# Optimization experiments

Hardware: AMD Instinct MI355X
Metric: run time of the kernel (lower is better)

The kernel has to match this reference:

```python
import jax, jax.numpy as jnp
import numpy as np

N = 50000   # nodes
E = 800000  # edges (avg degree 16)
D = 128     # in_channels == out_channels == edge_dim
BN_EPS = 1e-5
LN_EPS = 1e-5


def setup_inputs() -> dict:
    key = jax.random.key(0)
    ks = jax.random.split(key, 8)
    s = 0.05
    return {
        "x": jax.random.normal(ks[0], (N, D), jnp.float32),
        "edge_index": jax.random.randint(ks[1], (2, E), 0, N, dtype=jnp.int64),
        "edge_attr": jax.random.normal(ks[2], (E, D), jnp.float32),
        "eps": jnp.zeros((), jnp.float32),                       # GINE train_eps init 0
        "We": jax.random.normal(ks[3], (D, D), jnp.float32) * s,  # edge lin: edge_dim -> in_channels
        "be": jnp.zeros((D,), jnp.float32),
        "W1": jax.random.normal(ks[4], (D, D), jnp.float32) * s,  # mlp first linear
        "b1": jnp.zeros((D,), jnp.float32),
        "bn_g": jnp.ones((D,), jnp.float32),
        "bn_b": jnp.zeros((D,), jnp.float32),
        "bn_rm": jnp.zeros((D,), jnp.float32),  # running mean (eval mode)
        "bn_rv": jnp.ones((D,), jnp.float32),   # running var (eval mode)
        "W2": jax.random.normal(ks[5], (D, D), jnp.float32) * s,  # mlp second linear
        "b2": jnp.zeros((D,), jnp.float32),
        "ln_g": jnp.ones((D,), jnp.float32),
        "ln_b": jnp.zeros((D,), jnp.float32),
    }


def reference(x, edge_index, edge_attr, eps, We, be, W1, b1,
              bn_g, bn_b, bn_rm, bn_rv, W2, b2, ln_g, ln_b):
    src, dst = edge_index[0], edge_index[1]  # PyG: message from x_j = x[src], aggregate at dst
    # GINE message: relu(x_j + Lin(edge_attr)); gather + elementwise
    msg = jax.nn.relu(x[src] + edge_attr @ We.T + be)            # [E, D]
    aggr = jax.ops.segment_sum(msg, dst, num_segments=N)         # scatter-sum -> [N, D]
    h = (1.0 + eps) * x + aggr
    # MLP: Linear -> BatchNorm1d (eval) -> ReLU -> (Dropout=id) -> Linear
    h = h @ W1.T + b1
    h = (h - bn_rm) * jax.lax.rsqrt(bn_rv + BN_EPS) * bn_g + bn_b
    h = jax.nn.relu(h)
    h = h @ W2.T + b2
    # LayerNorm over feature dim
    mu = jnp.mean(h, axis=-1, keepdims=True)
    var = jnp.mean(jnp.square(h - mu), axis=-1, keepdims=True)
    h = (h - mu) * jax.lax.rsqrt(var + LN_EPS) * ln_g + ln_b
    # residual (Identity since in==out) + relu; dropout is identity in eval
    return jax.nn.relu(h + x)
```

## Files before the change

kernel.cpp:

```cpp
#include <hip/hip_runtime.h>
#include <hip/hip_bf16.h>

#define D 128
#define LDK 136

typedef __bf16 bf16x8 __attribute__((ext_vector_type(8)));
typedef float  f32x4  __attribute__((ext_vector_type(4)));
typedef unsigned short u16;

__device__ __forceinline__ u16 f2bf(float f) {
    unsigned int u = __builtin_bit_cast(unsigned int, f);
    u = u + 0x7FFFu + ((u >> 16) & 1u);
    return (u16)(u >> 16);
}
__device__ __forceinline__ float bf2f(u16 h) {
    unsigned int u = ((unsigned int)h) << 16;
    return __builtin_bit_cast(float, u);
}
__device__ __forceinline__ unsigned int pk2(float lo, float hi) {
    return (unsigned int)f2bf(lo) | ((unsigned int)f2bf(hi) << 16);
}
__device__ __forceinline__ void cvt_store8(u16* dst, float4 a, float4 b) {
    uint4 v;
    v.x = pk2(a.x, a.y); v.y = pk2(a.z, a.w);
    v.z = pk2(b.x, b.y); v.w = pk2(b.z, b.w);
    *reinterpret_cast<uint4*>(dst) = v;
}
__device__ __forceinline__ void cvt_store8v(u16* dst, f32x4 a, f32x4 b) {
    uint4 v;
    v.x = pk2(a.x, a.y); v.y = pk2(a.z, a.w);
    v.z = pk2(b.x, b.y); v.w = pk2(b.z, b.w);
    *reinterpret_cast<uint4*>(dst) = v;
}
__device__ __forceinline__ bf16x8 cvt8r(f32x4 a, f32x4 b) {
    uint4 v;
    v.x = pk2(a.x, a.y); v.y = pk2(a.z, a.w);
    v.z = pk2(b.x, b.y); v.w = pk2(b.z, b.w);
    return __builtin_bit_cast(bf16x8, v);
}

__global__ __launch_bounds__(256)
void hist_kernel(const int* __restrict__ ei, int* __restrict__ counts, int E) {
    int e = blockIdx.x * 256 + threadIdx.x;
    if (e < E) atomicAdd(&counts[ei[E + e]], 1);
}

__global__ __launch_bounds__(256)
void scan_partial(const int* __restrict__ counts, int* __restrict__ bsum) {
    const int b = blockIdx.x, t = threadIdx.x;
    const int4 v = reinterpret_cast<const int4*>(counts + (size_t)b * 1024)[t];
    int s = v.x + v.y + v.z + v.w;
    #pragma unroll
    for (int off = 1; off < 64; off <<= 1) s += __shfl_xor(s, off);
    __shared__ int ws[4];
    if ((t & 63) == 0) ws[t >> 6] = s;
    __syncthreads();
    if (t == 0) bsum[b] = ws[0] + ws[1] + ws[2] + ws[3];
}
__global__ __launch_bounds__(256)
void scan_bsum(int* __restrict__ bsum, int nb) {
    const int t = threadIdx.x;
    int s = (t < nb) ? bsum[t] : 0;
    int inc = s;
    const int lane = t & 63;
    #pragma unroll
    for (int off = 1; off < 64; off <<= 1) {
        int v = __shfl_up(inc, off);
        if (lane >= off) inc += v;
    }
    __shared__ int ws[4];
    if (lane == 63) ws[t >> 6] = inc;
    __syncthreads();
    int woff = 0;
    for (int i = 0; i < (t >> 6); ++i) woff += ws[i];
    if (t < nb) bsum[t] = woff + inc - s;
}
__global__ __launch_bounds__(256)
void scan_emit(const int* __restrict__ counts, const int* __restrict__ bsum,
               int* __restrict__ offsets) {
    const int b = blockIdx.x, t = threadIdx.x;
    const int4 v = reinterpret_cast<const int4*>(counts + (size_t)b * 1024)[t];
    const int s = v.x + v.y + v.z + v.w;
    int inc = s;
    const int lane = t & 63;
    #pragma unroll
    for (int off = 1; off < 64; off <<= 1) {
        int u = __shfl_up(inc, off);
        if (lane >= off) inc += u;
    }
    __shared__ int ws[4];
    if (lane == 63) ws[t >> 6] = inc;
    __syncthreads();
    int woff = bsum[b];
    for (int i = 0; i < (t >> 6); ++i) woff += ws[i];
    int e0 = woff + inc - s;
    int4 o;
    o.x = e0; o.y = e0 + v.x; o.z = o.y + v.y; o.w = o.z + v.z;
    reinterpret_cast<int4*>(offsets + (size_t)b * 1024)[t] = o;
}

__global__ __launch_bounds__(256)
void scatter_kernel(const int* __restrict__ ei, int* __restrict__ off,
                    int4* __restrict__ rec, int E) {
    int e = blockIdx.x * 256 + threadIdx.x;
    if (e < E) {
        int s = ei[e];
        int d = ei[E + e];
        int p = atomicAdd(&off[d], 1);
        rec[p] = make_int4(e, s, d, 0);
    }
}

__global__ __launch_bounds__(256, 4)
void gine_edge_sorted(const float* __restrict__ x,
                      const float* __restrict__ ea,
                      const float* __restrict__ We,
                      const float* __restrict__ be,
                      const int4* __restrict__ rec,
                      float* __restrict__ aggr,
                      int E)
{
    __shared__ u16 buf[128][LDK];
    __shared__ int eid_lds[128];
    __shared__ int src_lds[128];
    __shared__ int dst_lds[128];

    const int tid = threadIdx.x;
    const int e0  = blockIdx.x * 128;

    {
        const int row = tid >> 1;
        const int c0  = (tid & 1) * 64;
        const float4* gw = reinterpret_cast<const float4*>(We + (size_t)row * D + c0);
        #pragma unroll
        for (int j = 0; j < 8; ++j) {
            float4 w0 = gw[2*j], w1 = gw[2*j+1];
            cvt_store8(&buf[row][c0 + 8*j], w0, w1);
        }
        if (tid < 128) {
            const int p = e0 + tid;
            if (p < E) {
                int4 r4 = rec[p];
                eid_lds[tid] = r4.x; src_lds[tid] = r4.y; dst_lds[tid] = r4.z;
            } else {
                eid_lds[tid] = 0; src_lds[tid] = 0; dst_lds[tid] = -1;
            }
        }
    }
    __syncthreads();

    const int wave = tid >> 6, lane = tid & 63;
    const int lhi = lane >> 4, llo = lane & 15;
    const int r0 = wave * 32;

    f32x4 acc[2][8];
    #pragma unroll
    for (int m = 0; m < 2; ++m)
        #pragma unroll
        for (int n = 0; n < 8; ++n) acc[m][n] = (f32x4){0.f, 0.f, 0.f, 0.f};

    const f32x4* pa = reinterpret_cast<const f32x4*>(ea + (size_t)eid_lds[r0 + llo] * D);
    const f32x4* pb = reinterpret_cast<const f32x4*>(ea + (size_t)eid_lds[r0 + 16 + llo] * D);

#define LOADG(G, KK) { const int f4_ = ((KK)*32 + lhi*8) >> 2;                 \
        G[0] = __builtin_nontemporal_load(pa + f4_);                           \
        G[1] = __builtin_nontemporal_load(pa + f4_ + 1);                       \
        G[2] = __builtin_nontemporal_load(pb + f4_);                           \
        G[3] = __builtin_nontemporal_load(pb + f4_ + 1); }
#define MFMAG(G, KK) { bf16x8 a0_ = cvt8r(G[0], G[1]);                         \
        bf16x8 a1_ = cvt8r(G[2], G[3]);                                        \
        const int k0_ = (KK)*32 + lhi*8;                                       \
        _Pragma("unroll")                                                      \
        for (int nf = 0; nf < 8; ++nf) {                                       \
            bf16x8 b_ = *reinterpret_cast<const bf16x8*>(&buf[nf*16 + llo][k0_]); \
            acc[0][nf] = __builtin_amdgcn_mfma_f32_16x16x32_bf16(a0_, b_, acc[0][nf], 0, 0, 0); \
            acc[1][nf] = __builtin_amdgcn_mfma_f32_16x16x32_bf16(a1_, b_, acc[1][nf], 0, 0, 0); \
        } }

    f32x4 gA[4], gB[4];
    LOADG(gA, 0); LOADG(gB, 1);
    MFMAG(gA, 0); LOADG(gA, 2);
    MFMAG(gB, 1); LOADG(gB, 3);
    MFMAG(gA, 2); MFMAG(gB, 3);
#undef LOADG
#undef MFMAG

    float bev[8];
    #pragma unroll
    for (int nf = 0; nf < 8; ++nf) bev[nf] = be[nf*16 + llo];

    __syncthreads();

    {
        const int row = tid >> 1;
        const int c0  = (tid & 1) * 64;
        const int s   = src_lds[row];
        const f32x4* gx = reinterpret_cast<const f32x4*>(x + (size_t)s * D + c0);
        f32x4 xa[8];
        #pragma unroll
        for (int j = 0; j < 8; ++j) xa[j] = gx[j];
        #pragma unroll
        for (int j = 0; j < 4; ++j)
            cvt_store8v(&buf[row][c0 + 8*j], xa[2*j], xa[2*j+1]);
        #pragma unroll
        for (int j = 0; j < 8; ++j) xa[j] = gx[8 + j];
        #pragma unroll
        for (int j = 0; j < 4; ++j)
            cvt_store8v(&buf[row][c0 + 32 + 8*j], xa[2*j], xa[2*j+1]);
    }
    __syncthreads();

    #pragma unroll
    for (int mf = 0; mf < 2; ++mf) {
        #pragma unroll
        for (int r = 0; r < 4; ++r) {
            const int row = r0 + mf*16 + lhi*4 + r;
            const bool valid = (e0 + row) < E;
            #pragma unroll
            for (int nf = 0; nf < 8; ++nf) {
                const int col = nf*16 + llo;
                const float v = acc[mf][nf][r] + bf2f(buf[row][col]) + bev[nf];
                buf[row][col] = valid ? f2bf(fmaxf(v, 0.0f)) : (u16)0;
            }
        }
    }
    __syncthreads();

    {
        const int c   = tid & 127;
        const int h   = tid >> 7;
        const int rlo = h * 64;
        float sum = 0.0f;
        int prev  = dst_lds[rlo];
        int start = rlo;
        #pragma unroll 4
        for (int r = rlo; r < rlo + 64; ++r) {
            const float v = bf2f(buf[r][c]);
            const int d = dst_lds[r];
            if (d != prev) {
                if (prev >= 0) {
                    float* p = &aggr[(size_t)prev * D + c];
                    if (start == rlo) atomicAdd(p, sum);
                    else              *p = sum;
                }
                sum = 0.0f; prev = d; start = r;
            }
            sum += v;
        }
        if (prev >= 0) atomicAdd(&aggr[(size_t)prev * D + c], sum);
    }
}

__global__ __launch_bounds__(256, 4)
void gine_edge(const float* __restrict__ x,
               const int* __restrict__ ei,
               const float* __restrict__ ea,
               const float* __restrict__ We,
               const float* __restrict__ be,
               float* __restrict__ aggr,
               int E)
{
    __shared__ u16 w_lds[128][LDK];
    __shared__ int sd_lds[2][128];

    const int tid = threadIdx.x;
    const int e0  = blockIdx.x * 128;

    {
        const int row = tid >> 1;
        const int c0  = (tid & 1) * 64;
        const float4* gw = reinterpret_cast<const float4*>(We + (size_t)row * D + c0);
        #pragma unroll
        for (int j = 0; j < 8; ++j) {
            float4 w0 = gw[2*j], w1 = gw[2*j+1];
            cvt_store8(&w_lds[row][c0 + 8*j], w0, w1);
        }
        const int r = tid & 127, which = tid >> 7;
        int erow = e0 + r;
        sd_lds[which][r] = (erow < E) ? ei[(size_t)which * E + erow] : 0;
    }
    __syncthreads();

    const int wave = tid >> 6, lane = tid & 63;
    const int lhi = lane >> 4, llo = lane & 15;
    const int r0 = wave * 32;

    f32x4 acc[2][8];
    #pragma unroll
    for (int m = 0; m < 2; ++m)
        #pragma unroll
        for (int n = 0; n < 8; ++n) acc[m][n] = (f32x4){0.f, 0.f, 0.f, 0.f};

    int ra = e0 + r0 + llo;      if (ra >= E) ra = E - 1;
    int rb = e0 + r0 + 16 + llo; if (rb >= E) rb = E - 1;
    const f32x4* pa = reinterpret_cast<const f32x4*>(ea + (size_t)ra * D);
    const f32x4* pb = reinterpret_cast<const f32x4*>(ea + (size_t)rb * D);

    #pragma unroll
    for (int kk = 0; kk < 4; ++kk) {
        const int k0 = kk * 32 + lhi * 8;
        const int f4 = k0 >> 2;
        f32x4 u0 = __builtin_nontemporal_load(pa + f4);
        f32x4 u1 = __builtin_nontemporal_load(pa + f4 + 1);
        f32x4 v0 = __builtin_nontemporal_load(pb + f4);
        f32x4 v1 = __builtin_nontemporal_load(pb + f4 + 1);
        bf16x8 a0 = cvt8r(u0, u1);
        bf16x8 a1 = cvt8r(v0, v1);
        #pragma unroll
        for (int nf = 0; nf < 8; ++nf) {
            bf16x8 b = *reinterpret_cast<const bf16x8*>(&w_lds[nf*16 + llo][k0]);
            acc[0][nf] = __builtin_amdgcn_mfma_f32_16x16x32_bf16(a0, b, acc[0][nf], 0, 0, 0);
            acc[1][nf] = __builtin_amdgcn_mfma_f32_16x16x32_bf16(a1, b, acc[1][nf], 0, 0, 0);
        }
    }

    float bev[8];
    #pragma unroll
    for (int nf = 0; nf < 8; ++nf) bev[nf] = be[nf*16 + llo];

    #pragma unroll
    for (int mf = 0; mf < 2; ++mf) {
        #pragma unroll
        for (int r = 0; r < 4; ++r) {
            const int row = r0 + mf*16 + lhi*4 + r;
            if (e0 + row >= E) continue;
            const int s = sd_lds[0][row];
            const int d = sd_lds[1][row];
            const float* xr  = x    + (size_t)s * D;
            float*      arow = aggr + (size_t)d * D;
            #pragma unroll
            for (int nf = 0; nf < 8; ++nf) {
                const int col = nf*16 + llo;
                float v = acc[mf][nf][r] + xr[col] + bev[nf];
                atomicAdd(&arow[col], fmaxf(v, 0.0f));
            }
        }
    }
}

__global__ __launch_bounds__(256, 2)
void gine_node(const float* __restrict__ x,
               const float* __restrict__ aggr,
               const float* __restrict__ epsp,
               const float* __restrict__ W1,
               const float* __restrict__ b1,
               const float* __restrict__ bn_g,
               const float* __restrict__ bn_b,
               const float* __restrict__ bn_rm,
               const float* __restrict__ bn_rv,
               const float* __restrict__ W2,
               const float* __restrict__ b2,
               const float* __restrict__ ln_g,
               const float* __restrict__ ln_b,
               float* __restrict__ out,
               int N)
{
    __shared__ u16 h_lds[128][LDK];
    __shared__ u16 w_lds[128][LDK];

    const int tid = threadIdx.x;
    const int n0  = blockIdx.x * 128;
    const float epf = 1.0f + epsp[0];

    {
        const int row = tid >> 1;
        const int c0  = (tid & 1) * 64;
        int nrow = n0 + row; if (nrow >= N) nrow = N - 1;
        const float4* gx = reinterpret_cast<const float4*>(x    + (size_t)nrow * D + c0);
        const float4* ga = reinterpret_cast<const float4*>(aggr + (size_t)nrow * D + c0);
        const float4* gw = reinterpret_cast<const float4*>(W1   + (size_t)row  * D + c0);
        #pragma unroll
        for (int j = 0; j < 8; ++j) {
            float4 xv0 = gx[2*j], xv1 = gx[2*j+1];
            float4 av0 = ga[2*j], av1 = ga[2*j+1];
            float4 h0, h1;
            h0.x = epf*xv0.x + av0.x; h0.y = epf*xv0.y + av0.y;
            h0.z = epf*xv0.z + av0.z; h0.w = epf*xv0.w + av0.w;
            h1.x = epf*xv1.x + av1.x; h1.y = epf*xv1.y + av1.y;
            h1.z = epf*xv1.z + av1.z; h1.w = epf*xv1.w + av1.w;
            cvt_store8(&h_lds[row][c0 + 8*j], h0, h1);
            float4 w0 = gw[2*j], w1 = gw[2*j+1];
            cvt_store8(&w_lds[row][c0 + 8*j], w0, w1);
        }
    }
    __syncthreads();

    const int wave = tid >> 6, lane = tid & 63;
    const int lhi = lane >> 4, llo = lane & 15;
    const int r0 = wave * 32;

    f32x4 acc[2][8];
    #pragma unroll
    for (int m = 0; m < 2; ++m)
        #pragma unroll
        for (int n = 0; n < 8; ++n) acc[m][n] = (f32x4){0.f, 0.f, 0.f, 0.f};

    #pragma unroll
    for (int kk = 0; kk < 4; ++kk) {
        const int k0 = kk * 32 + lhi * 8;
        bf16x8 a0 = *reinterpret_cast<const bf16x8*>(&h_lds[r0 + llo][k0]);
        bf16x8 a1 = *reinterpret_cast<const bf16x8*>(&h_lds[r0 + 16 + llo][k0]);
        #pragma unroll
        for (int nf = 0; nf < 8; ++nf) {
            bf16x8 b = *reinterpret_cast<const bf16x8*>(&w_lds[nf*16 + llo][k0]);
            acc[0][nf] = __builtin_amdgcn_mfma_f32_16x16x32_bf16(a0, b, acc[0][nf], 0, 0, 0);
            acc[1][nf] = __builtin_amdgcn_mfma_f32_16x16x32_bf16(a1, b, acc[1][nf], 0, 0, 0);
        }
    }

    float sc[8], bi[8], b2v[8], lgv[8], lbv[8];
    #pragma unroll
    for (int nf = 0; nf < 8; ++nf) {
        const int c = nf*16 + llo;
        const float s = bn_g[c] * rsqrtf(bn_rv[c] + 1e-5f);
        sc[nf]  = s;
        bi[nf]  = (b1[c] - bn_rm[c]) * s + bn_b[c];
        b2v[nf] = b2[c];
        lgv[nf] = ln_g[c];
        lbv[nf] = ln_b[c];
    }

    __syncthreads();

    #pragma unroll
    for (int mf = 0; mf < 2; ++mf) {
        #pragma unroll
        for (int r = 0; r < 4; ++r) {
            const int row = r0 + mf*16 + lhi*4 + r;
            #pragma unroll
            for (int nf = 0; nf < 8; ++nf) {
                const int col = nf*16 + llo;
                const float v = fmaxf(acc[mf][nf][r] * sc[nf] + bi[nf], 0.0f);
                h_lds[row][col] = f2bf(v);
            }
        }
    }
    {
        const int row = tid >> 1;
        const int c0  = (tid & 1) * 64;
        const float4* gw = reinterpret_cast<const float4*>(W2 + (size_t)row * D + c0);
        #pragma unroll
        for (int j = 0; j < 8; ++j) {
            float4 w0 = gw[2*j], w1 = gw[2*j+1];
            cvt_store8(&w_lds[row][c0 + 8*j], w0, w1);
        }
    }
    __syncthreads();

    f32x4 acc2[2][8];
    #pragma unroll
    for (int m = 0; m < 2; ++m)
        #pragma unroll
        for (int n = 0; n < 8; ++n) acc2[m][n] = (f32x4){0.f, 0.f, 0.f, 0.f};

    #pragma unroll
    for (int kk = 0; kk < 4; ++kk) {
        const int k0 = kk * 32 + lhi * 8;
        bf16x8 a0 = *reinterpret_cast<const bf16x8*>(&h_lds[r0 + llo][k0]);
        bf16x8 a1 = *reinterpret_cast<const bf16x8*>(&h_lds[r0 + 16 + llo][k0]);
        #pragma unroll
        for (int nf = 0; nf < 8; ++nf) {
            bf16x8 b = *reinterpret_cast<const bf16x8*>(&w_lds[nf*16 + llo][k0]);
            acc2[0][nf] = __builtin_amdgcn_mfma_f32_16x16x32_bf16(a0, b, acc2[0][nf], 0, 0, 0);
            acc2[1][nf] = __builtin_amdgcn_mfma_f32_16x16x32_bf16(a1, b, acc2[1][nf], 0, 0, 0);
        }
    }

    #pragma unroll
    for (int mf = 0; mf < 2; ++mf) {
        #pragma unroll
        for (int r = 0; r < 4; ++r) {
            float hv[8];
            float ssum = 0.f;
            #pragma unroll
            for (int nf = 0; nf < 8; ++nf) {
                const float v = acc2[mf][nf][r] + b2v[nf];
                hv[nf] = v; ssum += v;
            }
            ssum += __shfl_xor(ssum, 1); ssum += __shfl_xor(ssum, 2);
            ssum += __shfl_xor(ssum, 4); ssum += __shfl_xor(ssum, 8);
            const float mu = ssum * (1.0f/128.0f);
            float qs = 0.f;
            #pragma unroll
            for (int nf = 0; nf < 8; ++nf) { const float dd = hv[nf] - mu; qs += dd*dd; }
            qs += __shfl_xor(qs, 1); qs += __shfl_xor(qs, 2);
            qs += __shfl_xor(qs, 4); qs += __shfl_xor(qs, 8);
            const float rstd = rsqrtf(qs * (1.0f/128.0f) + 1e-5f);

            const int nrow = n0 + r0 + mf*16 + lhi*4 + r;
            if (nrow < N) {
                const float* xr   = x   + (size_t)nrow * D;
                float*       orow = out + (size_t)nrow * D;
                #pragma unroll
                for (int nf = 0; nf < 8; ++nf) {
                    const int col = nf*16 + llo;
                    const float v = (hv[nf] - mu) * rstd * lgv[nf] + lbv[nf] + xr[col];
                    orow[col] = fmaxf(v, 0.0f);
                }
            }
        }
    }
}

extern "C" void kernel_launch(void* const* d_in, const int* in_sizes, int n_in,
                              void* d_out, int out_size, void* d_ws, size_t ws_size,
                              hipStream_t stream) {
    const float* x     = (const float*)d_in[0];
    const int*   ei    = (const int*)d_in[1];
    const float* ea    = (const float*)d_in[2];
    const float* epsp  = (const float*)d_in[3];
    const float* We    = (const float*)d_in[4];
    const float* be    = (const float*)d_in[5];
    const float* W1    = (const float*)d_in[6];
    const float* b1    = (const float*)d_in[7];
    const float* bn_g  = (const float*)d_in[8];
    const float* bn_b  = (const float*)d_in[9];
    const float* bn_rm = (const float*)d_in[10];
    const float* bn_rv = (const float*)d_in[11];
    const float* W2    = (const float*)d_in[12];
    const float* b2    = (const float*)d_in[13];
    const float* ln_g  = (const float*)d_in[14];
    const float* ln_b  = (const float*)d_in[15];
    float* out = (float*)d_out;

    const int N = in_sizes[0] / D;
    const int E = in_sizes[2] / D;

    const size_t aggr_bytes = (size_t)N * D * sizeof(float);
    const size_t cnt_elems  = ((size_t)N + 1023) & ~(size_t)1023;
    const size_t cnt_bytes  = cnt_elems * sizeof(int);
    const size_t bsum_bytes = 1024;
    const size_t rec_bytes  = (size_t)E * sizeof(int4);
    const size_t need = aggr_bytes + 2 * cnt_bytes + bsum_bytes + rec_bytes;
    const int nsb = (int)(cnt_elems / 1024);

    char* wsb = (char*)d_ws;

    if (ws_size >= need && nsb <= 256) {
        float* aggr    = (float*)(wsb);
        int*   counts  = (int*)(wsb + aggr_bytes);
        int*   offsets = (int*)(wsb + aggr_bytes + cnt_bytes);
        int*   bsum    = (int*)(wsb + aggr_bytes + 2*cnt_bytes);
        int4*  rec     = (int4*)(wsb + aggr_bytes + 2*cnt_bytes + bsum_bytes);

        (void)hipMemsetAsync(aggr, 0, aggr_bytes, stream);
        (void)hipMemsetAsync(counts, 0, cnt_bytes, stream);

        const int tblocks = (E + 255) / 256;
        hist_kernel<<<tblocks, 256, 0, stream>>>(ei, counts, E);
        scan_partial<<<nsb, 256, 0, stream>>>(counts, bsum);
        scan_bsum<<<1, 256, 0, stream>>>(bsum, nsb);
        scan_emit<<<nsb, 256, 0, stream>>>(counts, bsum, offsets);
        scatter_kernel<<<tblocks, 256, 0, stream>>>(ei, offsets, rec, E);

        const int eblocks = (E + 127) / 128;
        gine_edge_sorted<<<eblocks, 256, 0, stream>>>(x, ea, We, be, rec, aggr, E);

        const int nblocks = (N + 127) / 128;
        gine_node<<<nblocks, 256, 0, stream>>>(x, aggr, epsp, W1, b1, bn_g, bn_b,
                                               bn_rm, bn_rv, W2, b2, ln_g, ln_b, out, N);
    } else {
        float* aggr = (ws_size >= aggr_bytes) ? (float*)d_ws : out;
        (void)hipMemsetAsync(aggr, 0, aggr_bytes, stream);
        const int eblocks = (E + 127) / 128;
        gine_edge<<<eblocks, 256, 0, stream>>>(x, ei, ea, We, be, aggr, E);
        const int nblocks = (N + 127) / 128;
        gine_node<<<nblocks, 256, 0, stream>>>(x, aggr, epsp, W1, b1, bn_g, bn_b,
                                               bn_rm, bn_rv, W2, b2, ln_g, ln_b, out, N);
    }
}
```

Before: 386.2 us.

## Permute edge_attr into dst-sorted bf16 buffer during scatter, stream it in edge kernel

```diff
diff --git a/kernel.cpp b/kernel.cpp
--- a/kernel.cpp
+++ b/kernel.cpp
@@ -6,6 +6,7 @@
 
 typedef __bf16 bf16x8 __attribute__((ext_vector_type(8)));
 typedef float  f32x4  __attribute__((ext_vector_type(4)));
+typedef unsigned int u32x4 __attribute__((ext_vector_type(4)));
 typedef unsigned short u16;
 
 __device__ __forceinline__ u16 f2bf(float f) {
@@ -33,7 +34,7 @@
     *reinterpret_cast<uint4*>(dst) = v;
 }
 __device__ __forceinline__ bf16x8 cvt8r(f32x4 a, f32x4 b) {
-    uint4 v;
+    u32x4 v;
     v.x = pk2(a.x, a.y); v.y = pk2(a.z, a.w);
     v.z = pk2(b.x, b.y); v.w = pk2(b.z, b.w);
     return __builtin_bit_cast(bf16x8, v);
@@ -97,6 +98,183 @@
     int4 o;
     o.x = e0; o.y = e0 + v.x; o.z = o.y + v.y; o.w = o.z + v.z;
     reinterpret_cast<int4*>(offsets + (size_t)b * 1024)[t] = o;
+}
+
+__global__ __launch_bounds__(256)
+void scatter_permute(const int* __restrict__ ei, int* __restrict__ off,
+                     const float* __restrict__ ea,
+                     int2* __restrict__ rec2, u16* __restrict__ ea_s, int E) {
+    __shared__ int p_lds[128];
+    const int tid = threadIdx.x;
+    const int e0  = blockIdx.x * 128;
+    if (tid < 128) {
+        const int e = e0 + tid;
+        if (e < E) {
+            const int s = ei[e];
+            const int d = ei[E + e];
+            const int p = atomicAdd(&off[d], 1);
+            p_lds[tid] = p;
+            rec2[p] = make_int2(s, d);
+        }
+    }
+    __syncthreads();
+    const int row = tid >> 1;
+    const int c0  = (tid & 1) * 64;
+    const int e   = e0 + row;
+    if (e < E) {
+        const int p = p_lds[row];
+        const f32x4* g = reinterpret_cast<const f32x4*>(ea + (size_t)e * D + c0);
+        u16* dst = ea_s + (size_t)p * D + c0;
+        f32x4 v[16];
+        #pragma unroll
+        for (int j = 0; j < 16; ++j) v[j] = __builtin_nontemporal_load(g + j);
+        #pragma unroll
+        for (int j = 0; j < 8; ++j) {
+            u32x4 w;
+            w.x = pk2(v[2*j].x,   v[2*j].y);   w.y = pk2(v[2*j].z,   v[2*j].w);
+            w.z = pk2(v[2*j+1].x, v[2*j+1].y); w.w = pk2(v[2*j+1].z, v[2*j+1].w);
+            __builtin_nontemporal_store(w, reinterpret_cast<u32x4*>(dst + 8*j));
+        }
+    }
+}
+
+__global__ __launch_bounds__(256, 4)
+void gine_edge_sorted2(const float* __restrict__ x,
+                       const u16* __restrict__ ea_s,
+                       const float* __restrict__ We,
+                       const float* __restrict__ be,
+                       const int2* __restrict__ rec2,
+                       float* __restrict__ aggr,
+                       int E)
+{
+    __shared__ u16 buf[128][LDK];
+    __shared__ int src_lds[128];
+    __shared__ int dst_lds[128];
+
+    const int tid = threadIdx.x;
+    const int e0  = blockIdx.x * 128;
+
+    {
+        const int row = tid >> 1;
+        const int c0  = (tid & 1) * 64;
+        const float4* gw = reinterpret_cast<const float4*>(We + (size_t)row * D + c0);
+        #pragma unroll
+        for (int j = 0; j < 8; ++j) {
+            float4 w0 = gw[2*j], w1 = gw[2*j+1];
+            cvt_store8(&buf[row][c0 + 8*j], w0, w1);
+        }
+        if (tid < 128) {
+            const int p = e0 + tid;
+            if (p < E) {
+                int2 r2 = rec2[p];
+                src_lds[tid] = r2.x; dst_lds[tid] = r2.y;
+            } else {
+                src_lds[tid] = 0; dst_lds[tid] = -1;
+            }
+        }
+    }
+    __syncthreads();
+
+    const int wave = tid >> 6, lane = tid & 63;
+    const int lhi = lane >> 4, llo = lane & 15;
+    const int r0 = wave * 32;
+
+    f32x4 acc[2][8];
+    #pragma unroll
+    for (int m = 0; m < 2; ++m)
+        #pragma unroll
+        for (int n = 0; n < 8; ++n) acc[m][n] = (f32x4){0.f, 0.f, 0.f, 0.f};
+
+    int ra = e0 + r0 + llo;      if (ra >= E) ra = E - 1;
+    int rb = e0 + r0 + 16 + llo; if (rb >= E) rb = E - 1;
+    const u16* pa_ = ea_s + (size_t)ra * D;
+    const u16* pb_ = ea_s + (size_t)rb * D;
+
+    u32x4 araw[2][4];
+    #pragma unroll
+    for (int kk = 0; kk < 4; ++kk) {
+        const int o = kk * 32 + lhi * 8;
+        araw[0][kk] = __builtin_nontemporal_load(reinterpret_cast<const u32x4*>(pa_ + o));
+        araw[1][kk] = __builtin_nontemporal_load(reinterpret_cast<const u32x4*>(pb_ + o));
+    }
+
+    #pragma unroll
+    for (int kk = 0; kk < 4; ++kk) {
+        const int k0 = kk * 32 + lhi * 8;
+        bf16x8 a0 = __builtin_bit_cast(bf16x8, araw[0][kk]);
+        bf16x8 a1 = __builtin_bit_cast(bf16x8, araw[1][kk]);
+        #pragma unroll
+        for (int nf = 0; nf < 8; ++nf) {
+            bf16x8 b = *reinterpret_cast<const bf16x8*>(&buf[nf*16 + llo][k0]);
+            acc[0][nf] = __builtin_amdgcn_mfma_f32_16x16x32_bf16(a0, b, acc[0][nf], 0, 0, 0);
+            acc[1][nf] = __builtin_amdgcn_mfma_f32_16x16x32_bf16(a1, b, acc[1][nf], 0, 0, 0);
+        }
+    }
+
+    float bev[8];
+    #pragma unroll
+    for (int nf = 0; nf < 8; ++nf) bev[nf] = be[nf*16 + llo];
+
+    __syncthreads();
+
+    {
+        const int row = tid >> 1;
+        const int c0  = (tid & 1) * 64;
+        const int s   = src_lds[row];
+        const f32x4* gx = reinterpret_cast<const f32x4*>(x + (size_t)s * D + c0);
+        f32x4 xa[8];
+        #pragma unroll
+        for (int j = 0; j < 8; ++j) xa[j] = gx[j];
+        #pragma unroll
+        for (int j = 0; j < 4; ++j)
+            cvt_store8v(&buf[row][c0 + 8*j], xa[2*j], xa[2*j+1]);
+        #pragma unroll
+        for (int j = 0; j < 8; ++j) xa[j] = gx[8 + j];
+        #pragma unroll
+        for (int j = 0; j < 4; ++j)
+            cvt_store8v(&buf[row][c0 + 32 + 8*j], xa[2*j], xa[2*j+1]);
+    }
+    __syncthreads();
+
+    #pragma unroll
+    for (int mf = 0; mf < 2; ++mf) {
+        #pragma unroll
+        for (int r = 0; r < 4; ++r) {
+            const int row = r0 + mf*16 + lhi*4 + r;
+            const bool valid = (e0 + row) < E;
+            #pragma unroll
+            for (int nf = 0; nf < 8; ++nf) {
+                const int col = nf*16 + llo;
+                const float v = acc[mf][nf][r] + bf2f(buf[row][col]) + bev[nf];
+                buf[row][col] = valid ? f2bf(fmaxf(v, 0.0f)) : (u16)0;
+            }
+        }
+    }
+    __syncthreads();
+
+    {
+        const int c   = tid & 127;
+        const int h   = tid >> 7;
+        const int rlo = h * 64;
+        float sum = 0.0f;
+        int prev  = dst_lds[rlo];
+        int start = rlo;
+        #pragma unroll 4
+        for (int r = rlo; r < rlo + 64; ++r) {
+            const float v = bf2f(buf[r][c]);
+            const int d = dst_lds[r];
+            if (d != prev) {
+                if (prev >= 0) {
+                    float* p = &aggr[(size_t)prev * D + c];
+                    if (start == rlo) atomicAdd(p, sum);
+                    else              *p = sum;
+                }
+                sum = 0.0f; prev = d; start = r;
+            }
+            sum += v;
+        }
+        if (prev >= 0) atomicAdd(&aggr[(size_t)prev * D + c], sum);
+    }
 }
 
 __global__ __launch_bounds__(256)
@@ -162,28 +340,23 @@
     const f32x4* pa = reinterpret_cast<const f32x4*>(ea + (size_t)eid_lds[r0 + llo] * D);
     const f32x4* pb = reinterpret_cast<const f32x4*>(ea + (size_t)eid_lds[r0 + 16 + llo] * D);
 
-#define LOADG(G, KK) { const int f4_ = ((KK)*32 + lhi*8) >> 2;                 \
-        G[0] = __builtin_nontemporal_load(pa + f4_);                           \
-        G[1] = __builtin_nontemporal_load(pa + f4_ + 1);                       \
-        G[2] = __builtin_nontemporal_load(pb + f4_);                           \
-        G[3] = __builtin_nontemporal_load(pb + f4_ + 1); }
-#define MFMAG(G, KK) { bf16x8 a0_ = cvt8r(G[0], G[1]);                         \
-        bf16x8 a1_ = cvt8r(G[2], G[3]);                                        \
-        const int k0_ = (KK)*32 + lhi*8;                                       \
-        _Pragma("unroll")                                                      \
-        for (int nf = 0; nf < 8; ++nf) {                                       \
-            bf16x8 b_ = *reinterpret_cast<const bf16x8*>(&buf[nf*16 + llo][k0_]); \
-            acc[0][nf] = __builtin_amdgcn_mfma_f32_16x16x32_bf16(a0_, b_, acc[0][nf], 0, 0, 0); \
-            acc[1][nf] = __builtin_amdgcn_mfma_f32_16x16x32_bf16(a1_, b_, acc[1][nf], 0, 0, 0); \
-        } }
-
-    f32x4 gA[4], gB[4];
-    LOADG(gA, 0); LOADG(gB, 1);
-    MFMAG(gA, 0); LOADG(gA, 2);
-    MFMAG(gB, 1); LOADG(gB, 3);
-    MFMAG(gA, 2); MFMAG(gB, 3);
-#undef LOADG
-#undef MFMAG
+    #pragma unroll
+    for (int kk = 0; kk < 4; ++kk) {
+        const int k0 = kk * 32 + lhi * 8;
+        const int f4 = k0 >> 2;
+        f32x4 u0 = __builtin_nontemporal_load(pa + f4);
+        f32x4 u1 = __builtin_nontemporal_load(pa + f4 + 1);
+        f32x4 v0 = __builtin_nontemporal_load(pb + f4);
+        f32x4 v1 = __builtin_nontemporal_load(pb + f4 + 1);
+        bf16x8 a0 = cvt8r(u0, u1);
+        bf16x8 a1 = cvt8r(v0, v1);
+        #pragma unroll
+        for (int nf = 0; nf < 8; ++nf) {
+            bf16x8 b = *reinterpret_cast<const bf16x8*>(&buf[nf*16 + llo][k0]);
+            acc[0][nf] = __builtin_amdgcn_mfma_f32_16x16x32_bf16(a0, b, acc[0][nf], 0, 0, 0);
+            acc[1][nf] = __builtin_amdgcn_mfma_f32_16x16x32_bf16(a1, b, acc[1][nf], 0, 0, 0);
+        }
+    }
 
     float bev[8];
     #pragma unroll
@@ -530,41 +703,62 @@
     const size_t cnt_elems  = ((size_t)N + 1023) & ~(size_t)1023;
     const size_t cnt_bytes  = cnt_elems * sizeof(int);
     const size_t bsum_bytes = 1024;
-    const size_t rec_bytes  = (size_t)E * sizeof(int4);
-    const size_t need = aggr_bytes + 2 * cnt_bytes + bsum_bytes + rec_bytes;
+    const size_t rec2_bytes = (size_t)E * sizeof(int2);
+    const size_t eas_bytes  = (size_t)E * D * sizeof(u16);
+    const size_t rec4_bytes = (size_t)E * sizeof(int4);
+    const size_t base       = aggr_bytes + 2 * cnt_bytes + bsum_bytes;
+    const size_t need_full  = base + rec2_bytes + eas_bytes;
+    const size_t need_mid   = base + rec4_bytes;
     const int nsb = (int)(cnt_elems / 1024);
 
     char* wsb = (char*)d_ws;
-
-    if (ws_size >= need && nsb <= 256) {
+    const int tblocks = (E + 255) / 256;
+    const int eblocks = (E + 127) / 128;
+    const int nblocks = (N + 127) / 128;
+
+    if (ws_size >= need_full && nsb <= 256) {
         float* aggr    = (float*)(wsb);
         int*   counts  = (int*)(wsb + aggr_bytes);
         int*   offsets = (int*)(wsb + aggr_bytes + cnt_bytes);
         int*   bsum    = (int*)(wsb + aggr_bytes + 2*cnt_bytes);
-        int4*  rec     = (int4*)(wsb + aggr_bytes + 2*cnt_bytes + bsum_bytes);
+        int2*  rec2    = (int2*)(wsb + base);
+        u16*   ea_s    = (u16*)(wsb + base + rec2_bytes);
 
         (void)hipMemsetAsync(aggr, 0, aggr_bytes, stream);
         (void)hipMemsetAsync(counts, 0, cnt_bytes, stream);
 
-        const int tblocks = (E + 255) / 256;
+        hist_kernel<<<tblocks, 256, 0, stream>>>(ei, counts, E);
+        scan_partial<<<nsb, 256, 0, stream>>>(counts, bsum);
+        scan_bsum<<<1, 256, 0, stream>>>(bsum, nsb);
+        scan_emit<<<nsb, 256, 0, stream>>>(counts, bsum, offsets);
+        scatter_permute<<<eblocks, 256, 0, stream>>>(ei, offsets, ea, rec2, ea_s, E);
+
+        gine_edge_sorted2<<<eblocks, 256, 0, stream>>>(x, ea_s, We, be, rec2, aggr, E);
+        gine_node<<<nblocks, 256, 0, stream>>>(x, aggr, epsp, W1, b1, bn_g, bn_b,
+                                               bn_rm, bn_rv, W2, b2, ln_g, ln_b, out, N);
+    } else if (ws_size >= need_mid && nsb <= 256) {
+        float* aggr    = (float*)(wsb);
+        int*   counts  = (int*)(wsb + aggr_bytes);
+        int*   offsets = (int*)(wsb + aggr_bytes + cnt_bytes);
+        int*   bsum    = (int*)(wsb + aggr_bytes + 2*cnt_bytes);
+        int4*  rec     = (int4*)(wsb + base);
+
+        (void)hipMemsetAsync(aggr, 0, aggr_bytes, stream);
+        (void)hipMemsetAsync(counts, 0, cnt_bytes, stream);
+
         hist_kernel<<<tblocks, 256, 0, stream>>>(ei, counts, E);
         scan_partial<<<nsb, 256, 0, stream>>>(counts, bsum);
         scan_bsum<<<1, 256, 0, stream>>>(bsum, nsb);
         scan_emit<<<nsb, 256, 0, stream>>>(counts, bsum, offsets);
         scatter_kernel<<<tblocks, 256, 0, stream>>>(ei, offsets, rec, E);
 
-        const int eblocks = (E + 127) / 128;
         gine_edge_sorted<<<eblocks, 256, 0, stream>>>(x, ea, We, be, rec, aggr, E);
-
-        const int nblocks = (N + 127) / 128;
         gine_node<<<nblocks, 256, 0, stream>>>(x, aggr, epsp, W1, b1, bn_g, bn_b,
                                                bn_rm, bn_rv, W2, b2, ln_g, ln_b, out, N);
     } else {
         float* aggr = (ws_size >= aggr_bytes) ? (float*)d_ws : out;
         (void)hipMemsetAsync(aggr, 0, aggr_bytes, stream);
-        const int eblocks = (E + 127) / 128;
         gine_edge<<<eblocks, 256, 0, stream>>>(x, ei, ea, We, be, aggr, E);
-        const int nblocks = (N + 127) / 128;
         gine_node<<<nblocks, 256, 0, stream>>>(x, aggr, epsp, W1, b1, bn_g, bn_b,
                                                bn_rm, bn_rv, W2, b2, ln_g, ln_b, out, N);
     }
```

After: 1.186 ms. +207.2%, slower.

## Make sorted edge kernel persistent with resident weights and early x gather

Applied to the files above, without the earlier changes.

```diff
diff --git a/kernel.cpp b/kernel.cpp
--- a/kernel.cpp
+++ b/kernel.cpp
@@ -6,6 +6,7 @@
 
 typedef __bf16 bf16x8 __attribute__((ext_vector_type(8)));
 typedef float  f32x4  __attribute__((ext_vector_type(4)));
+typedef unsigned int u32x4 __attribute__((ext_vector_type(4)));
 typedef unsigned short u16;
 
 __device__ __forceinline__ u16 f2bf(float f) {
@@ -33,7 +34,7 @@
     *reinterpret_cast<uint4*>(dst) = v;
 }
 __device__ __forceinline__ bf16x8 cvt8r(f32x4 a, f32x4 b) {
-    uint4 v;
+    u32x4 v;
     v.x = pk2(a.x, a.y); v.y = pk2(a.z, a.w);
     v.z = pk2(b.x, b.y); v.w = pk2(b.z, b.w);
     return __builtin_bit_cast(bf16x8, v);
@@ -44,7 +45,6 @@
     int e = blockIdx.x * 256 + threadIdx.x;
     if (e < E) atomicAdd(&counts[ei[E + e]], 1);
 }
-
 __global__ __launch_bounds__(256)
 void scan_partial(const int* __restrict__ counts, int* __restrict__ bsum) {
     const int b = blockIdx.x, t = threadIdx.x;
@@ -98,7 +98,6 @@
     o.x = e0; o.y = e0 + v.x; o.z = o.y + v.y; o.w = o.z + v.z;
     reinterpret_cast<int4*>(offsets + (size_t)b * 1024)[t] = o;
 }
-
 __global__ __launch_bounds__(256)
 void scatter_kernel(const int* __restrict__ ei, int* __restrict__ off,
                     int4* __restrict__ rec, int E) {
@@ -111,22 +110,25 @@
     }
 }
 
-__global__ __launch_bounds__(256, 4)
-void gine_edge_sorted(const float* __restrict__ x,
-                      const float* __restrict__ ea,
-                      const float* __restrict__ We,
-                      const float* __restrict__ be,
-                      const int4* __restrict__ rec,
-                      float* __restrict__ aggr,
-                      int E)
+__global__ __launch_bounds__(256, 2)
+void gine_edge_pers(const float* __restrict__ x,
+                    const float* __restrict__ ea,
+                    const float* __restrict__ We,
+                    const float* __restrict__ be,
+                    const int4* __restrict__ rec,
+                    float* __restrict__ aggr,
+                    int E, int ntiles)
 {
-    __shared__ u16 buf[128][LDK];
+    __shared__ u16 wbuf[128][LDK];
+    __shared__ u16 mbuf[128][LDK];
     __shared__ int eid_lds[128];
     __shared__ int src_lds[128];
     __shared__ int dst_lds[128];
 
     const int tid = threadIdx.x;
-    const int e0  = blockIdx.x * 128;
+    const int wave = tid >> 6, lane = tid & 63;
+    const int lhi = lane >> 4, llo = lane & 15;
+    const int r0 = wave * 32;
 
     {
         const int row = tid >> 1;
@@ -135,8 +137,20 @@
         #pragma unroll
         for (int j = 0; j < 8; ++j) {
             float4 w0 = gw[2*j], w1 = gw[2*j+1];
-            cvt_store8(&buf[row][c0 + 8*j], w0, w1);
-        }
+            cvt_store8(&wbuf[row][c0 + 8*j], w0, w1);
+        }
+    }
+    float bev[8];
+    #pragma unroll
+    for (int nf = 0; nf < 8; ++nf) bev[nf] = be[nf*16 + llo];
+    __syncthreads();
+
+    const int xrow = tid >> 1;
+    const int xc0  = (tid & 1) * 64;
+
+    for (int tile = blockIdx.x; tile < ntiles; tile += gridDim.x) {
+        const int e0 = tile * 128;
+
         if (tid < 128) {
             const int p = e0 + tid;
             if (p < E) {
@@ -146,21 +160,17 @@
                 eid_lds[tid] = 0; src_lds[tid] = 0; dst_lds[tid] = -1;
             }
         }
-    }
-    __syncthreads();
-
-    const int wave = tid >> 6, lane = tid & 63;
-    const int lhi = lane >> 4, llo = lane & 15;
-    const int r0 = wave * 32;
-
-    f32x4 acc[2][8];
-    #pragma unroll
-    for (int m = 0; m < 2; ++m)
-        #pragma unroll
-        for (int n = 0; n < 8; ++n) acc[m][n] = (f32x4){0.f, 0.f, 0.f, 0.f};
-
-    const f32x4* pa = reinterpret_cast<const f32x4*>(ea + (size_t)eid_lds[r0 + llo] * D);
-    const f32x4* pb = reinterpret_cast<const f32x4*>(ea + (size_t)eid_lds[r0 + 16 + llo] * D);
+        __syncthreads();
+
+        f32x4 acc[2][8];
+        #pragma unroll
+        for (int m = 0; m < 2; ++m)
+            #pragma unroll
+            for (int n = 0; n < 8; ++n) acc[m][n] = (f32x4){0.f, 0.f, 0.f, 0.f};
+
+        const f32x4* pa = reinterpret_cast<const f32x4*>(ea + (size_t)eid_lds[r0 + llo] * D);
+        const f32x4* pb = reinterpret_cast<const f32x4*>(ea + (size_t)eid_lds[r0 + 16 + llo] * D);
+        const f32x4* gx = reinterpret_cast<const f32x4*>(x + (size_t)src_lds[xrow] * D + xc0);
 
 #define LOADG(G, KK) { const int f4_ = ((KK)*32 + lhi*8) >> 2;                 \
         G[0] = __builtin_nontemporal_load(pa + f4_);                           \
@@ -172,82 +182,70 @@
         const int k0_ = (KK)*32 + lhi*8;                                       \
         _Pragma("unroll")                                                      \
         for (int nf = 0; nf < 8; ++nf) {                                       \
-            bf16x8 b_ = *reinterpret_cast<const bf16x8*>(&buf[nf*16 + llo][k0_]); \
+            bf16x8 b_ = *reinterpret_cast<const bf16x8*>(&wbuf[nf*16 + llo][k0_]); \
             acc[0][nf] = __builtin_amdgcn_mfma_f32_16x16x32_bf16(a0_, b_, acc[0][nf], 0, 0, 0); \
             acc[1][nf] = __builtin_amdgcn_mfma_f32_16x16x32_bf16(a1_, b_, acc[1][nf], 0, 0, 0); \
         } }
 
-    f32x4 gA[4], gB[4];
-    LOADG(gA, 0); LOADG(gB, 1);
-    MFMAG(gA, 0); LOADG(gA, 2);
-    MFMAG(gB, 1); LOADG(gB, 3);
-    MFMAG(gA, 2); MFMAG(gB, 3);
+        f32x4 gA[4], gB[4], xa[8];
+        LOADG(gA, 0); LOADG(gB, 1);
+        #pragma unroll
+        for (int j = 0; j < 8; ++j) xa[j] = gx[j];
+        MFMAG(gA, 0); LOADG(gA, 2);
+        MFMAG(gB, 1); LOADG(gB, 3);
+        MFMAG(gA, 2); MFMAG(gB, 3);
 #undef LOADG
 #undef MFMAG
 
-    float bev[8];
-    #pragma unroll
-    for (int nf = 0; nf < 8; ++nf) bev[nf] = be[nf*16 + llo];
-
-    __syncthreads();
-
-    {
-        const int row = tid >> 1;
-        const int c0  = (tid & 1) * 64;
-        const int s   = src_lds[row];
-        const f32x4* gx = reinterpret_cast<const f32x4*>(x + (size_t)s * D + c0);
-        f32x4 xa[8];
-        #pragma unroll
-        for (int j = 0; j < 8; ++j) xa[j] = gx[j];
         #pragma unroll
         for (int j = 0; j < 4; ++j)
-            cvt_store8v(&buf[row][c0 + 8*j], xa[2*j], xa[2*j+1]);
+            cvt_store8v(&mbuf[xrow][xc0 + 8*j], xa[2*j], xa[2*j+1]);
         #pragma unroll
         for (int j = 0; j < 8; ++j) xa[j] = gx[8 + j];
         #pragma unroll
         for (int j = 0; j < 4; ++j)
-            cvt_store8v(&buf[row][c0 + 32 + 8*j], xa[2*j], xa[2*j+1]);
-    }
-    __syncthreads();
-
-    #pragma unroll
-    for (int mf = 0; mf < 2; ++mf) {
-        #pragma unroll
-        for (int r = 0; r < 4; ++r) {
-            const int row = r0 + mf*16 + lhi*4 + r;
-            const bool valid = (e0 + row) < E;
+            cvt_store8v(&mbuf[xrow][xc0 + 32 + 8*j], xa[2*j], xa[2*j+1]);
+
+        #pragma unroll
+        for (int mf = 0; mf < 2; ++mf) {
             #pragma unroll
-            for (int nf = 0; nf < 8; ++nf) {
-                const int col = nf*16 + llo;
-                const float v = acc[mf][nf][r] + bf2f(buf[row][col]) + bev[nf];
-                buf[row][col] = valid ? f2bf(fmaxf(v, 0.0f)) : (u16)0;
-            }
-        }
-    }
-    __syncthreads();
-
-    {
-        const int c   = tid & 127;
-        const int h   = tid >> 7;
-        const int rlo = h * 64;
-        float sum = 0.0f;
-        int prev  = dst_lds[rlo];
-        int start = rlo;
-        #pragma unroll 4
-        for (int r = rlo; r < rlo + 64; ++r) {
-            const float v = bf2f(buf[r][c]);
-            const int d = dst_lds[r];
-            if (d != prev) {
-                if (prev >= 0) {
-                    float* p = &aggr[(size_t)prev * D + c];
-                    if (start == rlo) atomicAdd(p, sum);
-                    else              *p = sum;
+            for (int r = 0; r < 4; ++r) {
+                const int row = r0 + mf*16 + lhi*4 + r;
+                const bool valid = (e0 + row) < E;
+                #pragma unroll
+                for (int nf = 0; nf < 8; ++nf) {
+                    const int col = nf*16 + llo;
+                    const float v = acc[mf][nf][r] + bf2f(mbuf[row][col]) + bev[nf];
+                    mbuf[row][col] = valid ? f2bf(fmaxf(v, 0.0f)) : (u16)0;
                 }
-                sum = 0.0f; prev = d; start = r;
-            }
-            sum += v;
-        }
-        if (prev >= 0) atomicAdd(&aggr[(size_t)prev * D + c], sum);
+            }
+        }
+        __syncthreads();
+
+        {
+            const int c   = tid & 127;
+            const int h   = tid >> 7;
+            const int rlo = h * 64;
+            float sum = 0.0f;
+            int prev  = dst_lds[rlo];
+            int start = rlo;
+            #pragma unroll 4
+            for (int r = rlo; r < rlo + 64; ++r) {
+                const float v = bf2f(mbuf[r][c]);
+                const int d = dst_lds[r];
+                if (d != prev) {
+                    if (prev >= 0) {
+                        float* p = &aggr[(size_t)prev * D + c];
+                        if (start == rlo) atomicAdd(p, sum);
+                        else              *p = sum;
+                    }
+                    sum = 0.0f; prev = d; start = r;
+                }
+                sum += v;
+            }
+            if (prev >= 0) atomicAdd(&aggr[(size_t)prev * D + c], sum);
+        }
+        __syncthreads();
     }
 }
 
@@ -530,41 +528,41 @@
     const size_t cnt_elems  = ((size_t)N + 1023) & ~(size_t)1023;
     const size_t cnt_bytes  = cnt_elems * sizeof(int);
     const size_t bsum_bytes = 1024;
-    const size_t rec_bytes  = (size_t)E * sizeof(int4);
-    const size_t need = aggr_bytes + 2 * cnt_bytes + bsum_bytes + rec_bytes;
+    const size_t rec4_bytes = (size_t)E * sizeof(int4);
+    const size_t base       = aggr_bytes + 2 * cnt_bytes + bsum_bytes;
+    const size_t need_mid   = base + rec4_bytes;
     const int nsb = (int)(cnt_elems / 1024);
 
     char* wsb = (char*)d_ws;
-
-    if (ws_size >= need && nsb <= 256) {
+    const int tblocks = (E + 255) / 256;
+    const int eblocks = (E + 127) / 128;
+    const int nblocks = (N + 127) / 128;
+    const int ntiles  = (E + 127) / 128;
+    const int pblocks = (ntiles < 512) ? ntiles : 512;
+
+    if (ws_size >= need_mid && nsb <= 256) {
         float* aggr    = (float*)(wsb);
         int*   counts  = (int*)(wsb + aggr_bytes);
         int*   offsets = (int*)(wsb + aggr_bytes + cnt_bytes);
         int*   bsum    = (int*)(wsb + aggr_bytes + 2*cnt_bytes);
-        int4*  rec     = (int4*)(wsb + aggr_bytes + 2*cnt_bytes + bsum_bytes);
+        int4*  rec     = (int4*)(wsb + base);
 
         (void)hipMemsetAsync(aggr, 0, aggr_bytes, stream);
         (void)hipMemsetAsync(counts, 0, cnt_bytes, stream);
 
-        const int tblocks = (E + 255) / 256;
         hist_kernel<<<tblocks, 256, 0, stream>>>(ei, counts, E);
         scan_partial<<<nsb, 256, 0, stream>>>(counts, bsum);
         scan_bsum<<<1, 256, 0, stream>>>(bsum, nsb);
         scan_emit<<<nsb, 256, 0, stream>>>(counts, bsum, offsets);
         scatter_kernel<<<tblocks, 256, 0, stream>>>(ei, offsets, rec, E);
 
-        const int eblocks = (E + 127) / 128;
-        gine_edge_sorted<<<eblocks, 256, 0, stream>>>(x, ea, We, be, rec, aggr, E);
-
-        const int nblocks = (N + 127) / 128;
+        gine_edge_pers<<<pblocks, 256, 0, stream>>>(x, ea, We, be, rec, aggr, E, ntiles);
         gine_node<<<nblocks, 256, 0, stream>>>(x, aggr, epsp, W1, b1, bn_g, bn_b,
                                                bn_rm, bn_rv, W2, b2, ln_g, ln_b, out, N);
     } else {
         float* aggr = (ws_size >= aggr_bytes) ? (float*)d_ws : out;
         (void)hipMemsetAsync(aggr, 0, aggr_bytes, stream);
-        const int eblocks = (E + 127) / 128;
         gine_edge<<<eblocks, 256, 0, stream>>>(x, ei, ea, We, be, aggr, E);
-        const int nblocks = (N + 127) / 128;
         gine_node<<<nblocks, 256, 0, stream>>>(x, aggr, epsp, W1, b1, bn_g, bn_b,
                                                bn_rm, bn_rv, W2, b2, ln_g, ln_b, out, N);
     }
```

Measured after the change: 374.0 us. -3.2%, faster.
